# Kernel tuning notes

Measured on AMD Instinct MI355X. Metric: run time of the kernel, lower is better.

Reference implementation:

```python
import jax, jax.numpy as jnp
import numpy as np

B, CIN, HIN, WIN = 8192, 16, 6, 6
FM = 64                      # feature_maps
DK = FM // 2                 # 32
DV = FM // 2                 # 32
NH = FM // 2                 # 32 heads -> dkh = dvh = 1
OUT_CH = 5
HID = 128


def _conv2d(x, w, b, stride=1):
    # x: NCHW, w: OIHW, VALID padding (padding=(k-1)//2 = 0 for k=2)
    y = jax.lax.conv_general_dilated(
        x, w, window_strides=(stride, stride), padding='VALID',
        dimension_numbers=('NCHW', 'OIHW', 'NCHW'))
    return y + b[None, :, None, None]


def setup_inputs() -> dict:
    key = jax.random.key(0)
    ks = jax.random.split(key, 13)
    s = 0.1  # small init scale keeps softmax logits well-conditioned
    return {
        'x':      jax.random.normal(ks[0], (B, CIN, HIN, WIN), jnp.float32),
        # AugmentedConv: conv_out (out_channels - dv), qkv conv (2dk+dv), attn 1x1
        'conv_w': jax.random.normal(ks[1], (FM - DV, CIN, 2, 2), jnp.float32) * s,
        'conv_b': jax.random.normal(ks[2], (FM - DV,), jnp.float32) * s,
        'qkv_w':  jax.random.normal(ks[3], (2 * DK + DV, CIN, 2, 2), jnp.float32) * s,
        'qkv_b':  jax.random.normal(ks[4], (2 * DK + DV,), jnp.float32) * s,
        'attn_w': jax.random.normal(ks[5], (DV, DV, 1, 1), jnp.float32) * s,
        'attn_b': jax.random.normal(ks[6], (DV,), jnp.float32) * s,
        # DoubleDense: fm*5*5 -> hid -> hid//2 -> out
        'w1': jax.random.normal(ks[7], (HID, FM * 5 * 5), jnp.float32) * s,
        'b1': jax.random.normal(ks[8], (HID,), jnp.float32) * s,
        'w2': jax.random.normal(ks[9], (HID // 2, HID), jnp.float32) * s,
        'b2': jax.random.normal(ks[10], (HID // 2,), jnp.float32) * s,
        'w3': jax.random.normal(ks[11], (OUT_CH, HID // 2), jnp.float32) * s,
        'b3': jax.random.normal(ks[12], (OUT_CH,), jnp.float32) * s,
    }


def _forward(x, conv_w, conv_b, qkv_w, qkv_b, attn_w, attn_b, w1, b1, w2, b2, w3, b3):
    # ---- AugmentedConv ----
    conv_out = _conv2d(x, conv_w, conv_b)            # [B, FM-DV, 5, 5]
    qkv = _conv2d(x, qkv_w, qkv_b)                   # [B, 2DK+DV, 5, 5]
    b, _, h, w = qkv.shape
    q, k, v = jnp.split(qkv, [DK, 2 * DK], axis=1)
    dkh = DK // NH
    q = q * (dkh ** -0.5)
    flat_q = q.reshape(b, NH, dkh, h * w)            # [B, Nh, dkh, HW]
    flat_k = k.reshape(b, NH, dkh, h * w)
    flat_v = v.reshape(b, NH, DV // NH, h * w)
    # logits = q^T k over head-dim: [B, Nh, HW, HW]
    logits = jnp.einsum('bndi,bndj->bnij', flat_q, flat_k)
    weights = jax.nn.softmax(logits, axis=-1)
    # attn = weights @ v^T -> [B, Nh, HW, dvh]
    attn = jnp.einsum('bnij,bnjd->bnid', weights, flat_v.transpose(0, 1, 3, 2))
    # faithful to torch: raw reshape (B, Nh, dvh, H, W) then combine heads
    attn = attn.reshape(b, NH, DV // NH, h, w).reshape(b, DV, h, w)
    attn = _conv2d(attn, attn_w, attn_b)             # 1x1 conv
    y = jnp.concatenate([conv_out, attn], axis=1)    # [B, FM, 5, 5]
    # ---- ReLU + DoubleDense ----
    y = jax.nn.relu(y).reshape(b, -1)                # [B, FM*25]
    y = jax.nn.relu(y @ w1.T + b1)
    y = jax.nn.relu(y @ w2.T + b2)
    return y @ w3.T + b3                             # [B, OUT_CH]


def reference(x, conv_w, conv_b, qkv_w, qkv_b, attn_w, attn_b, w1, b1, w2, b2, w3, b3):
    return _forward(x, conv_w, conv_b, qkv_w, qkv_b, attn_w, attn_b,
                    w1, b1, w2, b2, w3, b3)
```

## Files before the change

kernel.cpp:

```cpp
#include <hip/hip_runtime.h>
#include <hip/hip_bf16.h>
#include <cstdint>
#include <cstddef>


typedef __attribute__((ext_vector_type(4))) float f32x4;
typedef __attribute__((ext_vector_type(2))) float f32x2;
typedef __attribute__((ext_vector_type(8))) __bf16 bf16x8;
typedef __attribute__((ext_vector_type(4))) __bf16 bf16x4;

#define LOG2E 1.4426950408889634f
#define ACT_STRIDE 1608
#define ACT_LDS_BYTES (16 * ACT_STRIDE * 2)
#define SCRATCH_PER_WAVE 3456
#define LDS_TOTAL (ACT_LDS_BYTES + 8 * SCRATCH_PER_WAVE)

__device__ __forceinline__ float fast_exp2(float x) {
#if __has_builtin(__builtin_amdgcn_exp2f)
  return __builtin_amdgcn_exp2f(x);
#else
  return __expf(x * 0.6931471805599453f);
#endif
}

__device__ __forceinline__ f32x4 mfma16(bf16x8 a, bf16x8 b, f32x4 c) {
  return __builtin_amdgcn_mfma_f32_16x16x32_bf16(a, b, c, 0, 0, 0);
}

__device__ __forceinline__ unsigned pack2(float lo, float hi) {
  unsigned short a = __builtin_bit_cast(unsigned short, __float2bfloat16(lo));
  unsigned short b = __builtin_bit_cast(unsigned short, __float2bfloat16(hi));
  return ((unsigned)b << 16) | (unsigned)a;
}

__device__ __forceinline__ float bsel(int u, unsigned lsh) {
  return __builtin_bit_cast(float, (((unsigned)u) << lsh) & 0xffff0000u);
}

__global__ __launch_bounds__(64) void prep(
    const float* __restrict__ conv_w, const float* __restrict__ conv_b,
    const float* __restrict__ qkv_w,  const float* __restrict__ qkv_b,
    const float* __restrict__ attn_w,
    const float* __restrict__ w1, const float* __restrict__ w2,
    __hip_bfloat16* __restrict__ wqb, float* __restrict__ biasb,
    __hip_bfloat16* __restrict__ wab,
    __hip_bfloat16* __restrict__ w1bp, __hip_bfloat16* __restrict__ w2b) {
  const int t = threadIdx.x, tb = blockIdx.x;
  if (tb < 16) {
#pragma unroll
    for (int j = 0; j < 8; ++j) {
      int i = tb * 512 + j * 64 + t;
      float w = (i < 2048) ? conv_w[i] : qkv_w[i - 2048];
      if (i >= 4096 && i < 6144) w *= LOG2E;
      wqb[i] = __float2bfloat16(w);
    }
  } else if (tb == 16) {
#pragma unroll
    for (int j = 0; j < 16; ++j) wab[j * 64 + t] = __float2bfloat16(attn_w[j * 64 + t]);
    for (int i = t; i < 128; i += 64) {
      float b = (i < 32) ? conv_b[i] : qkv_b[i - 32];
      if (i >= 64 && i < 96) b *= LOG2E;
      biasb[i] = b;
    }
  } else if (tb < 145) {
    const int u = tb - 17;
    __shared__ float rowf[1600];
    const float* wr = w1 + u * 1600;
#pragma unroll
    for (int j = 0; j < 25; ++j) rowf[j * 64 + t] = wr[j * 64 + t];
    __hip_bfloat16* wo = w1bp + u * 1600;
#pragma unroll
    for (int j = 0; j < 25; ++j) {
      wo[j * 64 + t] = __float2bfloat16(rowf[t * 25 + j]);
    }
  } else {
#pragma unroll
    for (int j = 0; j < 64; ++j) {
      int i = (tb - 145) * 4096 + j * 64 + t;
      w2b[i] = __float2bfloat16(w2[i]);
    }
  }
}

__global__ __launch_bounds__(512) void kf(
    const float* __restrict__ x,
    const float* __restrict__ biasb,
    const __hip_bfloat16* __restrict__ wqb,
    const __hip_bfloat16* __restrict__ wab, const float* __restrict__ attn_b,
    const __hip_bfloat16* __restrict__ w1bp, const float* __restrict__ b1,
    const __hip_bfloat16* __restrict__ w2b, const float* __restrict__ b2,
    const float* __restrict__ w3, const float* __restrict__ b3,
    float* __restrict__ out) {
  extern __shared__ __align__(16) char lds_all[];
  const int t = threadIdx.x & 63;
  const int wv = threadIdx.x >> 6;
  const int l15 = t & 15, quad = t >> 4;

  __hip_bfloat16* act_lds = (__hip_bfloat16*)lds_all;
  char* my = lds_all + ACT_LDS_BYTES + wv * SCRATCH_PER_WAVE;
  __bf16* qs  = (__bf16*)my;
  __bf16* xs  = (__bf16*)(my + 1792);
  __bf16* as_ = (__bf16*)(my + 1792);

  const int b_base = blockIdx.x * 16 + wv * 2;
  const int n = t & 31, half = t >> 5;
  const int i0 = half * 12;
  const int bp0 = (n & 15) * 4;
  const unsigned lsh = (n & 16) ? 0u : 16u;

  float xr[9];
  {
    const float* xb = x + (size_t)b_base * 576;
#pragma unroll
    for (int i = 0; i < 9; ++i) xr[i] = xb[t + i * 64];
  }

#pragma unroll 1
  for (int it = 0; it < 2; ++it) {
    const int rowoff = (wv * 2 + it) * ACT_STRIDE;

#pragma unroll
    for (int i = 0; i < 9; ++i) xs[t + i * 64] = __float2bfloat16(xr[i]);

    unsigned pkK[2][4], pkV[2][4];
#pragma unroll
    for (int mt = 0; mt < 2; ++mt) {
      bf16x8 af[2];
      {
        int row = mt * 16 + l15;
        int pos = row < 24 ? row : 24;
        int ii = pos / 5, jj = pos - ii * 5;
        const __bf16* xp = xs + ii * 6 + jj;
#pragma unroll
        for (int ks = 0; ks < 2; ++ks) {
          const __bf16* p0 = xp + (ks * 8 + quad * 2) * 36;
          bf16x8 a;
          a[0] = p0[0];  a[1] = p0[1];  a[2] = p0[6];  a[3] = p0[7];
          a[4] = p0[36]; a[5] = p0[37]; a[6] = p0[42]; a[7] = p0[43];
          af[ks] = a;
        }
      }
#pragma unroll
      for (int nh = 0; nh < 2; ++nh) {
        bf16x8 bf4[4][2];
#pragma unroll
        for (int nt4 = 0; nt4 < 4; ++nt4)
#pragma unroll
          for (int ks = 0; ks < 2; ++ks)
            bf4[nt4][ks] = *(const bf16x8*)((const __bf16*)wqb +
                            ((nh * 4 + nt4) * 16 + l15) * 64 + ks * 32 + quad * 8);
        float bs[4];
#pragma unroll
        for (int nt4 = 0; nt4 < 4; ++nt4) bs[nt4] = biasb[(nh * 4 + nt4) * 16 + l15];

        f32x4 acc[4];
#pragma unroll
        for (int nt4 = 0; nt4 < 4; ++nt4) acc[nt4] = (f32x4){0.f, 0.f, 0.f, 0.f};
#pragma unroll
        for (int ks = 0; ks < 2; ++ks)
#pragma unroll
          for (int nt4 = 0; nt4 < 4; ++nt4)
            acc[nt4] = mfma16(af[ks], bf4[nt4][ks], acc[nt4]);

        if (nh == 0) {
#pragma unroll
          for (int r = 0; r < 4; ++r) {
            int orow = mt * 16 + quad * 4 + r;
            if (orow < 25) {
              act_lds[rowoff + orow * 64 + 0 * 16 + l15] =
                  __float2bfloat16(fmaxf(acc[0][r] + bs[0], 0.f));
              act_lds[rowoff + orow * 64 + 1 * 16 + l15] =
                  __float2bfloat16(fmaxf(acc[1][r] + bs[1], 0.f));
              qs[(0 * 16 + l15) * 28 + orow] = __float2bfloat16(acc[2][r] + bs[2]);
              qs[(1 * 16 + l15) * 28 + orow] = __float2bfloat16(acc[3][r] + bs[3]);
            }
          }
        } else {
#pragma unroll
          for (int r = 0; r < 4; ++r) {
            pkK[mt][r] = pack2(acc[0][r] + bs[0], acc[1][r] + bs[1]);
            pkV[mt][r] = pack2(acc[2][r] + bs[2], acc[3][r] + bs[3]);
          }
        }
      }
    }

    if (it == 0) {
      const float* xb = x + (size_t)(b_base + 1) * 576;
#pragma unroll
      for (int i = 0; i < 9; ++i) xr[i] = xb[t + i * 64];
    }

    f32x2 kl2[12], vv2[12];
#pragma unroll
    for (int c = 0; c < 12; ++c) {
      const int j0 = 2 * c, j1 = 2 * c + 1;
      int uk0 = __builtin_amdgcn_ds_bpermute(bp0 + 64 * ((j0 >> 2) & 3), (int)pkK[j0 >> 4][j0 & 3]);
      int uk1 = __builtin_amdgcn_ds_bpermute(bp0 + 64 * ((j1 >> 2) & 3), (int)pkK[j1 >> 4][j1 & 3]);
      int uv0 = __builtin_amdgcn_ds_bpermute(bp0 + 64 * ((j0 >> 2) & 3), (int)pkV[j0 >> 4][j0 & 3]);
      int uv1 = __builtin_amdgcn_ds_bpermute(bp0 + 64 * ((j1 >> 2) & 3), (int)pkV[j1 >> 4][j1 & 3]);
      kl2[c] = (f32x2){bsel(uk0, lsh), bsel(uk1, lsh)};
      vv2[c] = (f32x2){bsel(uv0, lsh), bsel(uv1, lsh)};
    }
    const float kl24 = bsel(__builtin_amdgcn_ds_bpermute(bp0 + 128, (int)pkK[1][0]), lsh);
    const float vv24 = bsel(__builtin_amdgcn_ds_bpermute(bp0 + 128, (int)pkV[1][0]), lsh);

    {
      const __bf16* qp = qs + n * 28 + i0;
      float qcur = (float)qp[0];
#pragma unroll 1
      for (int z = 0; z < 13; ++z) {
        const float qi = qcur;
        qcur = (float)qp[z + 1];
        const f32x2 qi2 = {qi, qi};
        f32x2 sA = {0.f, 0.f}, sB = {0.f, 0.f};
        f32x2 oA = {0.f, 0.f}, oB = {0.f, 0.f};
        float s4 = 0.f, o4 = 0.f;
#pragma unroll
        for (int p = 0; p < 6; ++p) {
          f32x2 mA = qi2 * kl2[p];
          f32x2 mB = qi2 * kl2[p + 6];
          f32x2 eA = {fast_exp2(mA.x), fast_exp2(mA.y)};
          f32x2 eB = {fast_exp2(mB.x), fast_exp2(mB.y)};
          sA += eA;
          sB += eB;
          oA = eA * vv2[p] + oA;
          oB = eB * vv2[p + 6] + oB;
        }
        {
          float e = fast_exp2(qi * kl24);
          s4 += e;
          o4 = __builtin_fmaf(e, vv24, o4);
        }
        float ss = ((sA.x + sA.y) + (sB.x + sB.y)) + s4;
        float oo = ((oA.x + oA.y) + (oB.x + oB.y)) + o4;
        as_[(i0 + z) * 32 + n] = __float2bfloat16(oo * __builtin_amdgcn_rcpf(ss));
      }
    }

    {
      bf16x8 bw[2]; float ab[2];
#pragma unroll
      for (int nt2 = 0; nt2 < 2; ++nt2) {
        int nn = nt2 * 16 + l15;
        bw[nt2] = *(const bf16x8*)((const __bf16*)wab + nn * 32 + quad * 8);
        ab[nt2] = attn_b[nn];
      }
#pragma unroll
      for (int mt = 0; mt < 2; ++mt) {
        int row = mt * 16 + l15;
        int rc = row < 24 ? row : 24;
        bf16x8 af = *(const bf16x8*)(as_ + rc * 32 + quad * 8);
        f32x4 acc[2];
#pragma unroll
        for (int nt2 = 0; nt2 < 2; ++nt2)
          acc[nt2] = mfma16(af, bw[nt2], (f32x4){0.f, 0.f, 0.f, 0.f});
#pragma unroll
        for (int r = 0; r < 4; ++r) {
          int orow = mt * 16 + quad * 4 + r;
          if (orow < 25) {
#pragma unroll
            for (int nt2 = 0; nt2 < 2; ++nt2)
              act_lds[rowoff + orow * 64 + 32 + nt2 * 16 + l15] =
                  __float2bfloat16(fmaxf(acc[nt2][r] + ab[nt2], 0.f));
          }
        }
      }
    }
  }

  __syncthreads();

  const int wave = threadIdx.x >> 6;
  const int b0 = blockIdx.x * 16;

  __hip_bfloat16* C1s = (__hip_bfloat16*)(lds_all + ACT_LDS_BYTES);
  __hip_bfloat16* C2s = (__hip_bfloat16*)(lds_all + ACT_LDS_BYTES + 4352);

  {
    f32x4 acc0 = {0.f, 0.f, 0.f, 0.f};
    f32x4 acc1 = {0.f, 0.f, 0.f, 0.f};
    const __bf16* aL   = (const __bf16*)act_lds + l15 * ACT_STRIDE + quad * 8;
    const __bf16* bptr = (const __bf16*)w1bp + (size_t)(wave * 16 + l15) * 1600 + quad * 8;
#pragma unroll 5
    for (int k0 = 0; k0 < 1600; k0 += 64) {
      acc0 = mfma16(*(const bf16x8*)(aL + k0),      *(const bf16x8*)(bptr + k0),      acc0);
      acc1 = mfma16(*(const bf16x8*)(aL + k0 + 32), *(const bf16x8*)(bptr + k0 + 32), acc1);
    }
    const int col = wave * 16 + l15;
    const float bias1 = b1[col];
#pragma unroll
    for (int r = 0; r < 4; ++r) {
      C1s[(quad * 4 + r) * 136 + col] =
          __float2bfloat16(fmaxf(acc0[r] + acc1[r] + bias1, 0.f));
    }
  }
  __syncthreads();

  if (wave < 4) {
    f32x4 acc2 = {0.f, 0.f, 0.f, 0.f};
    const __bf16* aL = (const __bf16*)C1s + l15 * 136 + quad * 8;
    const __bf16* bL = (const __bf16*)w2b + (wave * 16 + l15) * 128 + quad * 8;
#pragma unroll
    for (int k0 = 0; k0 < 128; k0 += 32)
      acc2 = mfma16(*(const bf16x8*)(aL + k0), *(const bf16x8*)(bL + k0), acc2);
    const int col = wave * 16 + l15;
    const float bias = b2[col];
#pragma unroll
    for (int r = 0; r < 4; ++r)
      C2s[(quad * 4 + r) * 72 + col] = __float2bfloat16(fmaxf(acc2[r] + bias, 0.f));
  }
  __syncthreads();

  if (threadIdx.x < 80) {
    const int row = threadIdx.x / 5;
    const int oc = threadIdx.x - row * 5;
    float s = b3[oc];
#pragma unroll
    for (int k = 0; k < 64; ++k)
      s += __bfloat162float(C2s[row * 72 + k]) * w3[oc * 64 + k];
    out[(size_t)(b0 + row) * 5 + oc] = s;
  }
}

extern "C" void kernel_launch(void* const* d_in, const int* in_sizes, int n_in,
                              void* d_out, int out_size, void* d_ws, size_t ws_size,
                              hipStream_t stream) {
  const float* x      = (const float*)d_in[0];
  const float* conv_w = (const float*)d_in[1];
  const float* conv_b = (const float*)d_in[2];
  const float* qkv_w  = (const float*)d_in[3];
  const float* qkv_b  = (const float*)d_in[4];
  const float* attn_w = (const float*)d_in[5];
  const float* attn_b = (const float*)d_in[6];
  const float* w1 = (const float*)d_in[7];
  const float* b1 = (const float*)d_in[8];
  const float* w2 = (const float*)d_in[9];
  const float* b2 = (const float*)d_in[10];
  const float* w3 = (const float*)d_in[11];
  const float* b3 = (const float*)d_in[12];
  float* out = (float*)d_out;

  char* ws = (char*)d_ws;
  __hip_bfloat16* w1bp  = (__hip_bfloat16*)ws;
  __hip_bfloat16* w2b   = (__hip_bfloat16*)(ws + 409600);
  __hip_bfloat16* wqb   = (__hip_bfloat16*)(ws + 425984);
  float*          biasb = (float*)(ws + 442368);
  __hip_bfloat16* wab   = (__hip_bfloat16*)(ws + 442880);

  hipFuncSetAttribute(reinterpret_cast<const void*>(kf),
                      hipFuncAttributeMaxDynamicSharedMemorySize, LDS_TOTAL);

  prep<<<dim3(147), dim3(64), 0, stream>>>(conv_w, conv_b, qkv_w, qkv_b, attn_w,
                                           w1, w2, wqb, biasb, wab, w1bp, w2b);
  kf<<<dim3(512), dim3(512), LDS_TOTAL, stream>>>(x, biasb, wqb, wab, attn_b,
                                                  w1bp, b1, w2b, b2, w3, b3, out);
}
```

Baseline: 156.4 us.

## Halve block size to 8 samples, doubling grid and per-wave dense tile width

Each block now handles 8 samples with 4 waves instead of 16 samples with 8 waves, giving 1024 blocks. The dense-layer MFMA stage is reworked so that each wave covers 32 output columns with two 16-wide tiles. Only 8 of the 16 MFMA rows are valid, so half of the dense-layer MFMA work is wasted padding. The aim is more blocks per CU and less LDS per block, for better occupancy and load balance across the 256 CUs, at the cost of reading the w1 weights from L2 twice as often per sample.

After: 164.3 us. 5.0% more time.

```diff
diff --git a/kernel.cpp b/kernel.cpp
--- a/kernel.cpp
+++ b/kernel.cpp
@@ -11,9 +11,9 @@
 
 #define LOG2E 1.4426950408889634f
 #define ACT_STRIDE 1608
-#define ACT_LDS_BYTES (16 * ACT_STRIDE * 2)
+#define ACT_LDS_BYTES (8 * ACT_STRIDE * 2)
 #define SCRATCH_PER_WAVE 3456
-#define LDS_TOTAL (ACT_LDS_BYTES + 8 * SCRATCH_PER_WAVE)
+#define LDS_TOTAL (ACT_LDS_BYTES + 4 * SCRATCH_PER_WAVE)
 
 __device__ __forceinline__ float fast_exp2(float x) {
 #if __has_builtin(__builtin_amdgcn_exp2f)
@@ -82,7 +82,7 @@
   }
 }
 
-__global__ __launch_bounds__(512) void kf(
+__global__ __launch_bounds__(256) void kf(
     const float* __restrict__ x,
     const float* __restrict__ biasb,
     const __hip_bfloat16* __restrict__ wqb,
@@ -102,7 +102,7 @@
   __bf16* xs  = (__bf16*)(my + 1792);
   __bf16* as_ = (__bf16*)(my + 1792);
 
-  const int b_base = blockIdx.x * 16 + wv * 2;
+  const int b_base = blockIdx.x * 8 + wv * 2;
   const int n = t & 31, half = t >> 5;
   const int i0 = half * 12;
   const int bp0 = (n & 15) * 4;
@@ -272,34 +272,48 @@
   __syncthreads();
 
   const int wave = threadIdx.x >> 6;
-  const int b0 = blockIdx.x * 16;
+  const int b0 = blockIdx.x * 8;
+  const int arow = l15 & 7;
 
   __hip_bfloat16* C1s = (__hip_bfloat16*)(lds_all + ACT_LDS_BYTES);
-  __hip_bfloat16* C2s = (__hip_bfloat16*)(lds_all + ACT_LDS_BYTES + 4352);
+  __hip_bfloat16* C2s = (__hip_bfloat16*)(lds_all + ACT_LDS_BYTES + 2176);
 
   {
-    f32x4 acc0 = {0.f, 0.f, 0.f, 0.f};
-    f32x4 acc1 = {0.f, 0.f, 0.f, 0.f};
-    const __bf16* aL   = (const __bf16*)act_lds + l15 * ACT_STRIDE + quad * 8;
-    const __bf16* bptr = (const __bf16*)w1bp + (size_t)(wave * 16 + l15) * 1600 + quad * 8;
+    f32x4 acc[2][2];
+#pragma unroll
+    for (int ct = 0; ct < 2; ++ct)
+#pragma unroll
+      for (int ks = 0; ks < 2; ++ks) acc[ct][ks] = (f32x4){0.f, 0.f, 0.f, 0.f};
+    const __bf16* aL    = (const __bf16*)act_lds + arow * ACT_STRIDE + quad * 8;
+    const __bf16* bptr0 = (const __bf16*)w1bp + (size_t)(wave * 32 + l15) * 1600 + quad * 8;
+    const __bf16* bptr1 = bptr0 + 16 * 1600;
 #pragma unroll 5
     for (int k0 = 0; k0 < 1600; k0 += 64) {
-      acc0 = mfma16(*(const bf16x8*)(aL + k0),      *(const bf16x8*)(bptr + k0),      acc0);
-      acc1 = mfma16(*(const bf16x8*)(aL + k0 + 32), *(const bf16x8*)(bptr + k0 + 32), acc1);
-    }
-    const int col = wave * 16 + l15;
-    const float bias1 = b1[col];
-#pragma unroll
-    for (int r = 0; r < 4; ++r) {
-      C1s[(quad * 4 + r) * 136 + col] =
-          __float2bfloat16(fmaxf(acc0[r] + acc1[r] + bias1, 0.f));
+      bf16x8 av0 = *(const bf16x8*)(aL + k0);
+      bf16x8 av1 = *(const bf16x8*)(aL + k0 + 32);
+      acc[0][0] = mfma16(av0, *(const bf16x8*)(bptr0 + k0),      acc[0][0]);
+      acc[0][1] = mfma16(av1, *(const bf16x8*)(bptr0 + k0 + 32), acc[0][1]);
+      acc[1][0] = mfma16(av0, *(const bf16x8*)(bptr1 + k0),      acc[1][0]);
+      acc[1][1] = mfma16(av1, *(const bf16x8*)(bptr1 + k0 + 32), acc[1][1]);
+    }
+#pragma unroll
+    for (int ct = 0; ct < 2; ++ct) {
+      const int col = wave * 32 + ct * 16 + l15;
+      const float bias1 = b1[col];
+#pragma unroll
+      for (int r = 0; r < 4; ++r) {
+        const int row = quad * 4 + r;
+        if (row < 8)
+          C1s[row * 136 + col] =
+              __float2bfloat16(fmaxf(acc[ct][0][r] + acc[ct][1][r] + bias1, 0.f));
+      }
     }
   }
   __syncthreads();
 
-  if (wave < 4) {
+  {
     f32x4 acc2 = {0.f, 0.f, 0.f, 0.f};
-    const __bf16* aL = (const __bf16*)C1s + l15 * 136 + quad * 8;
+    const __bf16* aL = (const __bf16*)C1s + arow * 136 + quad * 8;
     const __bf16* bL = (const __bf16*)w2b + (wave * 16 + l15) * 128 + quad * 8;
 #pragma unroll
     for (int k0 = 0; k0 < 128; k0 += 32)
@@ -307,12 +321,15 @@
     const int col = wave * 16 + l15;
     const float bias = b2[col];
 #pragma unroll
-    for (int r = 0; r < 4; ++r)
-      C2s[(quad * 4 + r) * 72 + col] = __float2bfloat16(fmaxf(acc2[r] + bias, 0.f));
+    for (int r = 0; r < 4; ++r) {
+      const int row = quad * 4 + r;
+      if (row < 8)
+        C2s[row * 72 + col] = __float2bfloat16(fmaxf(acc2[r] + bias, 0.f));
+    }
   }
   __syncthreads();
 
-  if (threadIdx.x < 80) {
+  if (threadIdx.x < 40) {
     const int row = threadIdx.x / 5;
     const int oc = threadIdx.x - row * 5;
     float s = b3[oc];
@@ -353,6 +370,6 @@
 
   prep<<<dim3(147), dim3(64), 0, stream>>>(conv_w, conv_b, qkv_w, qkv_b, attn_w,
                                            w1, w2, wqb, biasb, wab, w1bp, w2b);
-  kf<<<dim3(512), dim3(512), LDS_TOTAL, stream>>>(x, biasb, wqb, wab, attn_b,
-                                                  w1bp, b1, w2b, b2, w3, b3, out);
-}
+  kf<<<dim3(1024), dim3(256), LDS_TOTAL, stream>>>(x, biasb, wqb, wab, attn_b,
+                                                   w1bp, b1, w2b, b2, w3, b3, out);
+}
```
